# Performance work log

Measured on AMD Instinct MI355X. Metric: run time of the kernel, lower is better.

Reference implementation:

```python
import jax, jax.numpy as jnp
import numpy as np

B, T, D, U = 64, 512, 1024, 128


def setup_inputs() -> dict:
    key = jax.random.key(0)
    ks = jax.random.split(key, 6)
    inputs = jax.random.normal(ks[0], (B, T, D), dtype=jnp.float32)
    # left-aligned boolean mask from random sequence lengths in [T//2, T]
    lengths = jax.random.randint(ks[1], (B,), T // 2, T + 1)
    mask = jnp.arange(T)[None, :] < lengths[:, None]  # [B, T] bool
    kernel = jax.random.normal(ks[2], (D, U), dtype=jnp.float32) / np.sqrt(D).astype(np.float32)
    bias = jnp.zeros((U,), dtype=jnp.float32)
    chain_kernel = jax.random.normal(ks[3], (U, U), dtype=jnp.float32) * 0.1
    # boundary_initializer='zeros' in the module; use small randn so the path is exercised
    left_boundary = jax.random.normal(ks[4], (U,), dtype=jnp.float32) * 0.1
    right_boundary = jax.random.normal(ks[5], (U,), dtype=jnp.float32) * 0.1
    return dict(inputs=inputs, mask=mask, kernel=kernel, bias=bias,
                chain_kernel=chain_kernel, left_boundary=left_boundary,
                right_boundary=right_boundary)


def _add_boundary_energy(potentials, mask, start, end):
    # start energy where mask turns on, end energy where mask turns off (tfa semantics)
    right_shift = jnp.pad(mask[:, :-1], ((0, 0), (1, 0)))  # mask shifted right by 1
    left_shift = jnp.pad(mask[:, 1:], ((0, 0), (0, 1)))    # mask shifted left by 1
    start_mask = (mask & ~right_shift)[..., None].astype(potentials.dtype)  # [B,T,1]
    end_mask = (mask & ~left_shift)[..., None].astype(potentials.dtype)     # [B,T,1]
    return potentials + start_mask * start[None, None, :] + end_mask * end[None, None, :]


def _viterbi_decode(potentials, chain_kernel, mask):
    # potentials: [B,T,U], chain_kernel: [U,U], mask: [B,T] bool (left-aligned)
    Uz = potentials.shape[-1]
    iota = jnp.arange(Uz)

    def fwd_step(state, xs):
        pot_t, m_t = xs                                    # [B,U], [B]
        scores = state[:, :, None] + chain_kernel[None]    # [B,U_prev,U_next]
        bp = jnp.argmax(scores, axis=1)                    # [B,U]
        new_state = pot_t + jnp.max(scores, axis=1)        # [B,U]
        m = m_t[:, None]
        state = jnp.where(m, new_state, state)             # carry state past padding
        bp = jnp.where(m, bp, iota[None, :])               # identity backpointer on padding
        return state, bp

    init = potentials[:, 0]
    xs = (jnp.swapaxes(potentials[:, 1:], 0, 1), mask[:, 1:].T)
    final_state, bps = jax.lax.scan(fwd_step, init, xs)    # bps: [T-1,B,U]
    last_tag = jnp.argmax(final_state, axis=-1)            # [B]

    def back_step(tag, bp):
        prev = jnp.take_along_axis(bp, tag[:, None], axis=1)[:, 0]
        return prev, tag

    first_tag, tags_rest = jax.lax.scan(back_step, last_tag, bps, reverse=True)
    return jnp.concatenate([first_tag[:, None], tags_rest.T], axis=1)  # [B,T] int32


def reference(inputs, mask, kernel, bias, chain_kernel, left_boundary, right_boundary):
    # unary potentials via the internal Dense(units) (use_kernel=True)
    potentials = jnp.einsum('btd,du->btu', inputs, kernel) + bias
    # boundary energies (use_boundary=True)
    potentials = _add_boundary_energy(potentials, mask, left_boundary, right_boundary)
    # Viterbi decode (predict-phase output), one-hot as in the wrapper layer
    tags = _viterbi_decode(potentials, chain_kernel, mask)
    decoded_onehot = jax.nn.one_hot(tags, potentials.shape[-1], dtype=potentials.dtype)
    # train phase returns potentials, predict phase returns the one-hot decode;
    # return both so either path can be checked
    return potentials, decoded_onehot
```

## Files before the change

kernel.cpp:

```cpp
#include <hip/hip_runtime.h>
#include <cstdint>
#include <cstddef>

#define BB 64
#define TT 512
#define DD 1024
#define UU 128
#define MM (BB*TT)

__device__ __forceinline__ int mask_elem_bytes(const uint8_t* m) {
    return m[1] ? 1 : 4;
}
__device__ __forceinline__ int mask_at(const uint8_t* m, int eb, int idx) {
    return m[(size_t)idx * eb] != 0;
}

#define BM 64
#define KC 32

__global__ __launch_bounds__(256) void gemm_pot(
    const float* __restrict__ A, const float* __restrict__ Bw,
    const float* __restrict__ bias, const float* __restrict__ lb,
    const float* __restrict__ rb, const uint8_t* __restrict__ mask,
    float* __restrict__ out)
{
    __shared__ float As[KC][68];
    __shared__ float Bs[KC][132];

    const int tid = threadIdx.x;
    const int m0  = blockIdx.x * BM;
    const int rg  = tid >> 5;
    const int cg  = tid & 31;

    const int s_kg  = tid & 7;
    const int s_row = tid >> 3;
    const int b_c4  = tid & 31;
    const int b_kr0 = tid >> 5;

    float acc[8][4];
    #pragma unroll
    for (int r = 0; r < 8; ++r)
        #pragma unroll
        for (int e = 0; e < 4; ++e) acc[r][e] = 0.f;

    const float* aptr0 = A + (size_t)(m0 + s_row)      * DD + s_kg * 4;
    const float* aptr1 = A + (size_t)(m0 + s_row + 32) * DD + s_kg * 4;

    float4 a_pre0 = *(const float4*)(aptr0);
    float4 a_pre1 = *(const float4*)(aptr1);
    float4 b_pre[4];
    #pragma unroll
    for (int p = 0; p < 4; ++p)
        b_pre[p] = *(const float4*)(Bw + (size_t)(b_kr0 + p*8) * UU + b_c4*4);

    for (int k0 = 0; k0 < DD; k0 += KC) {
        __syncthreads();
        {
            const float av0[4] = {a_pre0.x, a_pre0.y, a_pre0.z, a_pre0.w};
            const float av1[4] = {a_pre1.x, a_pre1.y, a_pre1.z, a_pre1.w};
            #pragma unroll
            for (int e = 0; e < 4; ++e) {
                As[s_kg*4 + e][s_row]      = av0[e];
                As[s_kg*4 + e][s_row + 32] = av1[e];
            }
            #pragma unroll
            for (int p = 0; p < 4; ++p)
                *(float4*)&Bs[b_kr0 + p*8][b_c4*4] = b_pre[p];
        }
        __syncthreads();

        if (k0 + KC < DD) {
            a_pre0 = *(const float4*)(aptr0 + k0 + KC);
            a_pre1 = *(const float4*)(aptr1 + k0 + KC);
            #pragma unroll
            for (int p = 0; p < 4; ++p)
                b_pre[p] = *(const float4*)(Bw + (size_t)(k0 + KC + b_kr0 + p*8) * UU + b_c4*4);
        }

        #pragma unroll
        for (int kk = 0; kk < KC; ++kk) {
            float4 b4  = *(const float4*)&Bs[kk][cg*4];
            float4 a40 = *(const float4*)&As[kk][rg*8];
            float4 a41 = *(const float4*)&As[kk][rg*8 + 4];
            const float av[8] = {a40.x, a40.y, a40.z, a40.w, a41.x, a41.y, a41.z, a41.w};
            #pragma unroll
            for (int r = 0; r < 8; ++r) {
                acc[r][0] = fmaf(av[r], b4.x, acc[r][0]);
                acc[r][1] = fmaf(av[r], b4.y, acc[r][1]);
                acc[r][2] = fmaf(av[r], b4.z, acc[r][2]);
                acc[r][3] = fmaf(av[r], b4.w, acc[r][3]);
            }
        }
    }

    const float4 bias4 = *(const float4*)&bias[cg*4];
    const float4 lb4   = *(const float4*)&lb[cg*4];
    const float4 rb4   = *(const float4*)&rb[cg*4];
    const int eb = mask_elem_bytes(mask);

    #pragma unroll
    for (int r = 0; r < 8; ++r) {
        const int m  = m0 + rg*8 + r;
        const int bi = m >> 9;
        const int ti = m & 511;
        const int mt = mask_at(mask, eb, bi*TT + ti);
        const int mp = (ti > 0)      ? mask_at(mask, eb, bi*TT + ti - 1) : 0;
        const int mn = (ti < TT - 1) ? mask_at(mask, eb, bi*TT + ti + 1) : 0;
        const float sflag = (mt && !mp) ? 1.f : 0.f;
        const float eflag = (mt && !mn) ? 1.f : 0.f;
        float4 o;
        o.x = acc[r][0] + bias4.x + sflag*lb4.x + eflag*rb4.x;
        o.y = acc[r][1] + bias4.y + sflag*lb4.y + eflag*rb4.y;
        o.z = acc[r][2] + bias4.z + sflag*lb4.z + eflag*rb4.z;
        o.w = acc[r][3] + bias4.w + sflag*lb4.w + eflag*rb4.w;
        *(float4*)&out[(size_t)m*UU + cg*4] = o;
    }
}

template<bool STORE_MX>
__global__ __launch_bounds__(512) void viterbi_fwd(
    const float* __restrict__ pot, const uint8_t* __restrict__ mask,
    const float* __restrict__ chain, float* __restrict__ hist,
    float* __restrict__ mxb)
{
    const int b   = blockIdx.x;
    const int tid = threadIdx.x;
    const int seg = tid >> 7;
    const int j   = tid & 127;

    __shared__ float state_s[128];
    __shared__ float part[4][128];
    __shared__ int   wcnt[8];

    const int eb = mask_elem_bytes(mask);
    const int mm = mask_at(mask, eb, b*TT + tid);
    const unsigned long long bal = __ballot(mm);
    if ((tid & 63) == 0) wcnt[tid >> 6] = __popcll(bal);

    float cc[32];
    #pragma unroll
    for (int k = 0; k < 32; ++k) cc[k] = chain[(seg*32 + k)*UU + j];

    float potcur = 0.f, potnx = 0.f;
    if (tid < 128) {
        const float p0 = pot[(size_t)(b*TT)*UU + j];
        state_s[j] = p0;
        hist[(size_t)(b*TT)*UU + j] = p0;
        potcur = pot[(size_t)(b*TT + 1)*UU + j];
    }
    __syncthreads();

    int len = 0;
    #pragma unroll
    for (int w = 0; w < 8; ++w) len += wcnt[w];

    for (int t = 1; t < len; ++t) {
        float a0 = -3.4e38f, a1 = a0;
        const float4* sp = (const float4*)&state_s[seg*32];
        #pragma unroll
        for (int q = 0; q < 8; ++q) {
            const float4 s4 = sp[q];
            const float t0 = s4.x + cc[4*q + 0];
            const float t1 = s4.y + cc[4*q + 1];
            const float t2 = s4.z + cc[4*q + 2];
            const float t3 = s4.w + cc[4*q + 3];
            a0 = fmaxf(fmaxf(a0, t0), t1);
            a1 = fmaxf(fmaxf(a1, t2), t3);
        }
        part[seg][j] = fmaxf(a0, a1);
        if (tid < 128 && t + 1 < len)
            potnx = pot[(size_t)(b*TT + t + 1)*UU + j];
        __syncthreads();
        if (tid < 128) {
            const float mx = fmaxf(fmaxf(part[0][j], part[1][j]),
                                   fmaxf(part[2][j], part[3][j]));
            if (STORE_MX)
                mxb[((size_t)b*TT + t)*UU + j] = mx;
            const float ns = potcur + mx;
            state_s[j] = ns;
            hist[((size_t)b*TT + t)*UU + j] = ns;
            potcur = potnx;
        }
        __syncthreads();
    }
}

__global__ __launch_bounds__(64) void viterbi_bt_eq(
    const float* __restrict__ hist, const float* __restrict__ mxb,
    const uint8_t* __restrict__ mask, const float* __restrict__ chain,
    float* __restrict__ oh)
{
    const int b = blockIdx.x;
    const int l = threadIdx.x;

    __shared__ float ct[128][128];
    for (int r = 0; r < 256; ++r) {
        const int idx = r*64 + l;
        const int i = idx >> 7;
        const int j = idx & 127;
        ct[j][(i + j) & 127] = chain[i*UU + j];
    }

    const int eb = mask_elem_bytes(mask);
    int cnt = 0;
    #pragma unroll
    for (int e = 0; e < 8; ++e) cnt += mask_at(mask, eb, b*TT + e*64 + l);
    #pragma unroll
    for (int off = 32; off > 0; off >>= 1) cnt += __shfl_down(cnt, off);
    const int len = __shfl(cnt, 0);
    __syncthreads();

    const float* Hb = hist + (size_t)b*TT*UU;
    const float* Xb = mxb  + (size_t)b*TT*UU;

    const float v0 = Hb[(size_t)(len-1)*UU + l], v1 = Hb[(size_t)(len-1)*UU + l + 64];
    float mx = fmaxf(v0, v1);
    #pragma unroll
    for (int off = 32; off > 0; off >>= 1) mx = fmaxf(mx, __shfl_xor(mx, off));
    const unsigned long long c0 = __ballot(v0 == mx);
    const unsigned long long c1 = __ballot(v1 == mx);
    int tag = c0 ? __builtin_ctzll(c0) : 64 + __builtin_ctzll(c1);

    for (int t = len + l; t < TT; t += 64)
        oh[((size_t)b*TT + t)*UU + tag] = 1.0f;

    const int r2 = (len >= 2) ? len - 2 : 0;
    const int r3 = (len >= 3) ? len - 3 : 0;
    float hc0 = Hb[(size_t)r2*UU + l], hc1 = Hb[(size_t)r2*UU + l + 64];
    float hm0 = Hb[(size_t)r3*UU + l], hm1 = Hb[(size_t)r3*UU + l + 64];
    float xc0 = Xb[(size_t)(len-1)*UU + l], xc1 = Xb[(size_t)(len-1)*UU + l + 64];
    float xm0 = Xb[(size_t)r2*UU + l],      xm1 = Xb[(size_t)r2*UU + l + 64];

    for (int t = len - 1; t >= 1; --t) {
        if (l == 0) oh[((size_t)b*TT + t)*UU + tag] = 1.0f;

        const int th = (t >= 3) ? t - 3 : 0;
        const int tx = (t >= 2) ? t - 2 : 0;
        const float hf0 = Hb[(size_t)th*UU + l], hf1 = Hb[(size_t)th*UU + l + 64];
        const float xf0 = Xb[(size_t)tx*UU + l], xf1 = Xb[(size_t)tx*UU + l + 64];

        const float Va = __shfl(xc0, tag & 63);
        const float Vb = __shfl(xc1, tag & 63);
        const float V  = (tag < 64) ? Va : Vb;

        const float w0 = hc0 + ct[tag][(l + tag) & 127];
        const float w1 = hc1 + ct[tag][(l + 64 + tag) & 127];
        const unsigned long long b0 = __ballot(w0 == V);
        const unsigned long long b1 = __ballot(w1 == V);
        if (b0)      tag = __builtin_ctzll(b0);
        else if (b1) tag = 64 + __builtin_ctzll(b1);

        hc0 = hm0; hc1 = hm1; hm0 = hf0; hm1 = hf1;
        xc0 = xm0; xc1 = xm1; xm0 = xf0; xm1 = xf1;
    }
    if (l == 0) oh[((size_t)b*TT)*UU + tag] = 1.0f;
}

__global__ __launch_bounds__(64) void viterbi_bt(
    const float* __restrict__ hist, const uint8_t* __restrict__ mask,
    const float* __restrict__ chain, float* __restrict__ oh)
{
    const int b = blockIdx.x;
    const int l = threadIdx.x;

    __shared__ float ct[128][128];
    for (int r = 0; r < 256; ++r) {
        const int idx = r*64 + l;
        const int i = idx >> 7;
        const int j = idx & 127;
        ct[j][(i + j) & 127] = chain[i*UU + j];
    }

    const int eb = mask_elem_bytes(mask);
    int cnt = 0;
    #pragma unroll
    for (int e = 0; e < 8; ++e) cnt += mask_at(mask, eb, b*TT + e*64 + l);
    #pragma unroll
    for (int off = 32; off > 0; off >>= 1) cnt += __shfl_down(cnt, off);
    const int len = __shfl(cnt, 0);
    __syncthreads();

    const float* srow = &hist[((size_t)b*TT + (len - 1))*UU];
    const float v0 = srow[l], v1 = srow[l + 64];
    float mx = fmaxf(v0, v1);
    #pragma unroll
    for (int off = 32; off > 0; off >>= 1) mx = fmaxf(mx, __shfl_xor(mx, off));
    const unsigned long long c0 = __ballot(v0 == mx);
    const unsigned long long c1 = __ballot(v1 == mx);
    int tag = c0 ? __builtin_ctzll(c0) : 64 + __builtin_ctzll(c1);

    for (int t = len + l; t < TT; t += 64)
        oh[((size_t)b*TT + t)*UU + tag] = 1.0f;

    for (int t = len - 1; t >= 1; --t) {
        if (l == 0) oh[((size_t)b*TT + t)*UU + tag] = 1.0f;
        const float* sr = &hist[((size_t)b*TT + (t - 1))*UU];
        const float s0 = sr[l], s1 = sr[l + 64];
        const float w0 = s0 + ct[tag][(l + tag) & 127];
        const float w1 = s1 + ct[tag][(l + 64 + tag) & 127];
        float m2 = fmaxf(w0, w1);
        #pragma unroll
        for (int off = 32; off > 0; off >>= 1) m2 = fmaxf(m2, __shfl_xor(m2, off));
        const unsigned long long b0 = __ballot(w0 == m2);
        const unsigned long long b1 = __ballot(w1 == m2);
        tag = b0 ? __builtin_ctzll(b0) : 64 + __builtin_ctzll(b1);
    }
    if (l == 0) oh[((size_t)b*TT)*UU + tag] = 1.0f;
}

extern "C" void kernel_launch(void* const* d_in, const int* in_sizes, int n_in,
                              void* d_out, int out_size, void* d_ws, size_t ws_size,
                              hipStream_t stream)
{
    (void)in_sizes; (void)n_in; (void)out_size;
    const float*   inp   = (const float*)d_in[0];
    const uint8_t* mask  = (const uint8_t*)d_in[1];
    const float*   kern  = (const float*)d_in[2];
    const float*   bias  = (const float*)d_in[3];
    const float*   chain = (const float*)d_in[4];
    const float*   lb    = (const float*)d_in[5];
    const float*   rb    = (const float*)d_in[6];

    const size_t nel = (size_t)BB*TT*UU;
    float* pot  = (float*)d_out;
    float* oh   = pot + nel;
    float* hist = (float*)d_ws;
    float* mxb  = hist + nel;
    const bool eq_path = ws_size >= 2 * nel * sizeof(float);

    hipMemsetAsync(oh, 0, nel*sizeof(float), stream);
    gemm_pot<<<MM/BM, 256, 0, stream>>>(inp, kern, bias, lb, rb, mask, pot);
    if (eq_path) {
        viterbi_fwd<true><<<BB, 512, 0, stream>>>(pot, mask, chain, hist, mxb);
        viterbi_bt_eq<<<BB, 64, 0, stream>>>(hist, mxb, mask, chain, oh);
    } else {
        viterbi_fwd<false><<<BB, 512, 0, stream>>>(pot, mask, chain, hist, nullptr);
        viterbi_bt<<<BB, 64, 0, stream>>>(hist, mask, chain, oh);
    }
}
```

Before: 707.1 us.

## Use one barrier per Viterbi step with per-wave redundant state update

The forward Viterbi loop drops from two block-wide barriers per timestep to one. Every wave now redundantly reduces the four partial maxima and writes its own private copy of the next state. The state and partial buffers are double-buffered by timestep parity, so the second barrier is no longer needed to avoid read/write hazards. The cost is redundant reduction work and extra pot loads in all eight waves, plus relying on a raw s_barrier with an lgkmcnt wait instead of __syncthreads.

```diff
diff --git a/kernel.cpp b/kernel.cpp
--- a/kernel.cpp
+++ b/kernel.cpp
@@ -7,6 +7,9 @@
 #define DD 1024
 #define UU 128
 #define MM (BB*TT)
+
+#define WAVE_SYNC() do { asm volatile("s_waitcnt lgkmcnt(0)" ::: "memory"); \
+                         __builtin_amdgcn_s_barrier(); } while (0)
 
 __device__ __forceinline__ int mask_elem_bytes(const uint8_t* m) {
     return m[1] ? 1 : 4;
@@ -125,38 +128,45 @@
 {
     const int b   = blockIdx.x;
     const int tid = threadIdx.x;
+    const int w   = tid >> 6;
+    const int l   = tid & 63;
     const int seg = tid >> 7;
     const int j   = tid & 127;
 
-    __shared__ float state_s[128];
-    __shared__ float part[4][128];
+    __shared__ float st[8][2][128];
+    __shared__ float part[2][4][132];
     __shared__ int   wcnt[8];
 
     const int eb = mask_elem_bytes(mask);
     const int mm = mask_at(mask, eb, b*TT + tid);
     const unsigned long long bal = __ballot(mm);
-    if ((tid & 63) == 0) wcnt[tid >> 6] = __popcll(bal);
+    if (l == 0) wcnt[w] = __popcll(bal);
 
     float cc[32];
     #pragma unroll
     for (int k = 0; k < 32; ++k) cc[k] = chain[(seg*32 + k)*UU + j];
 
-    float potcur = 0.f, potnx = 0.f;
-    if (tid < 128) {
-        const float p0 = pot[(size_t)(b*TT)*UU + j];
-        state_s[j] = p0;
-        hist[(size_t)(b*TT)*UU + j] = p0;
-        potcur = pot[(size_t)(b*TT + 1)*UU + j];
-    }
+    const float* Pb = pot + (size_t)b*TT*UU;
+    float* Hb = hist + (size_t)b*TT*UU;
+    float* Xb = STORE_MX ? (mxb + (size_t)b*TT*UU) : nullptr;
+
+    {
+        const float p0 = Pb[l], p1 = Pb[l + 64];
+        st[w][0][l] = p0; st[w][0][l + 64] = p1;
+        if (w == 0) { Hb[l] = p0; Hb[l + 64] = p1; }
+    }
+    float potc0 = Pb[(size_t)UU + l], potc1 = Pb[(size_t)UU + l + 64];
     __syncthreads();
 
     int len = 0;
     #pragma unroll
-    for (int w = 0; w < 8; ++w) len += wcnt[w];
+    for (int q = 0; q < 8; ++q) len += wcnt[q];
 
     for (int t = 1; t < len; ++t) {
+        const int cur = (t - 1) & 1;
+
         float a0 = -3.4e38f, a1 = a0;
-        const float4* sp = (const float4*)&state_s[seg*32];
+        const float4* sp = (const float4*)&st[w][cur][seg*32];
         #pragma unroll
         for (int q = 0; q < 8; ++q) {
             const float4 s4 = sp[q];
@@ -167,21 +177,33 @@
             a0 = fmaxf(fmaxf(a0, t0), t1);
             a1 = fmaxf(fmaxf(a1, t2), t3);
         }
-        part[seg][j] = fmaxf(a0, a1);
-        if (tid < 128 && t + 1 < len)
-            potnx = pot[(size_t)(b*TT + t + 1)*UU + j];
-        __syncthreads();
-        if (tid < 128) {
-            const float mx = fmaxf(fmaxf(part[0][j], part[1][j]),
-                                   fmaxf(part[2][j], part[3][j]));
-            if (STORE_MX)
-                mxb[((size_t)b*TT + t)*UU + j] = mx;
-            const float ns = potcur + mx;
-            state_s[j] = ns;
-            hist[((size_t)b*TT + t)*UU + j] = ns;
-            potcur = potnx;
-        }
-        __syncthreads();
+        part[cur][seg][j] = fmaxf(a0, a1);
+
+        float pn0 = 0.f, pn1 = 0.f;
+        if (t + 1 < len) {
+            pn0 = Pb[(size_t)(t + 1)*UU + l];
+            pn1 = Pb[(size_t)(t + 1)*UU + l + 64];
+        }
+
+        WAVE_SYNC();
+
+        const float m0 = fmaxf(fmaxf(fmaxf(part[cur][0][l],      part[cur][1][l]),
+                                     part[cur][2][l]),      part[cur][3][l]);
+        const float m1 = fmaxf(fmaxf(fmaxf(part[cur][0][l + 64], part[cur][1][l + 64]),
+                                     part[cur][2][l + 64]), part[cur][3][l + 64]);
+        const float ns0 = potc0 + m0;
+        const float ns1 = potc1 + m1;
+        st[w][cur ^ 1][l]      = ns0;
+        st[w][cur ^ 1][l + 64] = ns1;
+        if (w == 0) {
+            Hb[(size_t)t*UU + l]      = ns0;
+            Hb[(size_t)t*UU + l + 64] = ns1;
+            if (STORE_MX) {
+                Xb[(size_t)t*UU + l]      = m0;
+                Xb[(size_t)t*UU + l + 64] = m1;
+            }
+        }
+        potc0 = pn0; potc1 = pn1;
     }
 }
 
```

Measured after the change: 704.4 us. Within noise of the previous version (-0.4%).
